# Optimization experiments

Hardware: AMD Instinct MI355X
Metric: run time of the kernel (lower is better)

Reference implementation:

```python
import jax, jax.numpy as jnp
import numpy as np

K = 64
M = 256
V = 5000

def setup_inputs() -> dict:
    key = jax.random.key(0)
    ks = jax.random.split(key, 8)
    feat_x = jax.random.normal(ks[0], (1, V, M), dtype=jnp.float32)
    feat_y = jax.random.normal(ks[1], (1, V, M), dtype=jnp.float32)
    evals_x = jnp.sort(jax.random.uniform(ks[2], (1, K), dtype=jnp.float32))
    evals_y = jnp.sort(jax.random.uniform(ks[3], (1, K), dtype=jnp.float32))
    evecs_trans_x = jax.random.normal(ks[4], (1, K, V), dtype=jnp.float32) / np.sqrt(V)
    evecs_trans_y = jax.random.normal(ks[5], (1, K, V), dtype=jnp.float32) / np.sqrt(V)
    eye = jnp.eye(K, dtype=jnp.float32)
    sqrtMk_x = (eye + 0.05 * jax.random.normal(ks[6], (K, K), dtype=jnp.float32))[None]
    sqrtMk_y = (eye + 0.05 * jax.random.normal(ks[7], (K, K), dtype=jnp.float32))[None]
    return {"feat_x": feat_x, "feat_y": feat_y, "evals_x": evals_x, "evals_y": evals_y,
            "evecs_trans_x": evecs_trans_x, "evecs_trans_y": evecs_trans_y,
            "sqrtMk_x": sqrtMk_x, "sqrtMk_y": sqrtMk_y}

LMBDA = 0.001

def _fmap(fx, fy, ex, ey, tx, ty, sx, sy):
    # squeeze batch dim of 1 (as in torch .squeeze())
    fx, fy = fx[0], fy[0]            # [V, m]
    ex, ey = ex[0], ey[0]            # [k]
    tx, ty = tx[0], ty[0]            # [k, V]
    sx, sy = sx[0], sy[0]            # [k, k]
    A = tx @ fx                      # [k, m] spectral coeffs of feat_x
    B = sy @ (ty @ fy)               # adapt_feature=True: premultiply by sqrtMk_y
    k, m = A.shape
    vec_B = B.T.reshape(m * k, 1)
    At_Ik = jnp.kron(A.T, sy)        # [m*k, k*k] (adapt_feature -> Ik = sqrtMk_y)
    first = At_Ik.T @ At_Ik          # [k^2, k^2]
    # adapt_mask=True branch
    inv_sx = jnp.linalg.inv(sx)
    lx = jnp.diag(ex)
    ly = jnp.diag(ey)
    lx_Ik = jnp.kron(lx @ inv_sx, sy)
    Ik_ly = jnp.kron(inv_sx, sy @ ly)
    Delta = lx_Ik - Ik_ly
    second = Delta.T @ Delta
    rhs = At_Ik.T @ vec_B
    op = first + LMBDA * second
    C = jnp.linalg.solve(op, rhs)
    return C.reshape(k, k).T[None]   # [1, k, k]

def reference(feat_x, feat_y, evals_x, evals_y, evecs_trans_x, evecs_trans_y, sqrtMk_x, sqrtMk_y):
    # bidirectional=False -> only Cxy (Cyx is None in the torch module)
    return _fmap(feat_x, feat_y, evals_x, evals_y, evecs_trans_x, evecs_trans_y, sqrtMk_x, sqrtMk_y)
```

## Files before the change

kernel.cpp:

```cpp
#include <hip/hip_runtime.h>

#define LMBDA 0.001f
#define NS_SY 4
#define NS_SX 5
#define OUTER_FULL 2
#define LDP 68
#define GYS 30

#define WS_A    0
#define WS_FY   16384
#define WS_G1   32768
#define WS_FYAT 36864
#define WS_T1   40960
#define WS_R2   45056
#define WS_R4   49152
#define WS_C    53248
#define WS_FLAGS 57344

#define FMA4(ar, xs, b) { ar[0]=fmaf((xs),(b).x,ar[0]); ar[1]=fmaf((xs),(b).y,ar[1]); \
                          ar[2]=fmaf((xs),(b).z,ar[2]); ar[3]=fmaf((xs),(b).w,ar[3]); }
#define COMP(v,q) ((q)==0?(v).x:((q)==1?(v).y:((q)==2?(v).z:(v).w)))

template<int SA, int SB>
__device__ __forceinline__ void mm64(const float* __restrict__ A,
                                     const float* __restrict__ B,
                                     int ti, int tj, float a[4][4]) {
    #pragma unroll 4
    for (int k = 0; k < 64; k += 4) {
        float4 av0 = *(const float4*)&A[(4 * ti + 0) * SA + k];
        float4 av1 = *(const float4*)&A[(4 * ti + 1) * SA + k];
        float4 av2 = *(const float4*)&A[(4 * ti + 2) * SA + k];
        float4 av3 = *(const float4*)&A[(4 * ti + 3) * SA + k];
        float4 b0 = *(const float4*)&B[(k + 0) * SB + 4 * tj];
        float4 b1 = *(const float4*)&B[(k + 1) * SB + 4 * tj];
        float4 b2 = *(const float4*)&B[(k + 2) * SB + 4 * tj];
        float4 b3 = *(const float4*)&B[(k + 3) * SB + 4 * tj];
        FMA4(a[0], av0.x, b0); FMA4(a[0], av0.y, b1); FMA4(a[0], av0.z, b2); FMA4(a[0], av0.w, b3);
        FMA4(a[1], av1.x, b0); FMA4(a[1], av1.y, b1); FMA4(a[1], av1.z, b2); FMA4(a[1], av1.w, b3);
        FMA4(a[2], av2.x, b0); FMA4(a[2], av2.y, b1); FMA4(a[2], av2.z, b2); FMA4(a[2], av2.w, b3);
        FMA4(a[3], av3.x, b0); FMA4(a[3], av3.y, b1); FMA4(a[3], av3.z, b2); FMA4(a[3], av3.w, b3);
    }
}

template<int SA, int SB>
__device__ __forceinline__ void mmdot(const float* __restrict__ A,
                                      const float* __restrict__ B,
                                      int ti, int tj, float a[4][4]) {
    #pragma unroll 4
    for (int m = 0; m < 64; m += 4) {
        float4 av[4], bv[4];
        #pragma unroll
        for (int r = 0; r < 4; ++r) av[r] = *(const float4*)&A[(4 * ti + r) * SA + m];
        #pragma unroll
        for (int c = 0; c < 4; ++c) bv[c] = *(const float4*)&B[(4 * tj + c) * SB + m];
        #pragma unroll
        for (int r = 0; r < 4; ++r)
            #pragma unroll
            for (int c = 0; c < 4; ++c)
                a[r][c] += av[r].x * bv[c].x + av[r].y * bv[c].y
                         + av[r].z * bv[c].z + av[r].w * bv[c].w;
    }
}

template<int SM>
__device__ __forceinline__ void ns_invert(const float* sM, float* sX, float* sY,
                                          int iters, int ti, int tj,
                                          int tid, float alpha)
{
    const float a2 = alpha * alpha;
    for (int idx = tid; idx < 4096; idx += 256) {
        int i = idx >> 6, j = idx & 63;
        sX[i * LDP + j] = ((i == j) ? 2.f * alpha : 0.f) - a2 * sM[i * SM + j];
    }
    __syncthreads();
    for (int it = 1; it < iters; ++it) {
        float y[4][4] = {};
        mm64<SM, LDP>(sM, sX, ti, tj, y);
        #pragma unroll
        for (int r = 0; r < 4; ++r) {
            float4 v = {y[r][0], y[r][1], y[r][2], y[r][3]};
            *(float4*)&sY[(4 * ti + r) * 64 + 4 * tj] = v;
        }
        __syncthreads();
        float z[4][4] = {};
        mm64<LDP, 64>(sX, sY, ti, tj, z);
        __syncthreads();
        #pragma unroll
        for (int r = 0; r < 4; ++r) {
            float4 xv = *(const float4*)&sX[(4 * ti + r) * LDP + 4 * tj];
            xv.x = 2.f * xv.x - z[r][0];
            xv.y = 2.f * xv.y - z[r][1];
            xv.z = 2.f * xv.z - z[r][2];
            xv.w = 2.f * xv.w - z[r][3];
            *(float4*)&sX[(4 * ti + r) * LDP + 4 * tj] = xv;
        }
        __syncthreads();
    }
}

template<bool DOR>
__device__ __forceinline__ void ns_pass(const float* Xs, const float* Rs,
                                        float* Xd, float* Rd, int ti, int tj)
{
    float xr[4][4] = {}, rr[4][4] = {};
    #pragma unroll 4
    for (int k = 0; k < 64; k += 4) {
        float4 xa[4], ra[4];
        #pragma unroll
        for (int r = 0; r < 4; ++r) {
            xa[r] = *(const float4*)&Xs[(4 * ti + r) * LDP + k];
            if (DOR) ra[r] = *(const float4*)&Rs[(4 * ti + r) * LDP + k];
        }
        #pragma unroll
        for (int q = 0; q < 4; ++q) {
            float4 bv = *(const float4*)&Rs[(k + q) * LDP + 4 * tj];
            #pragma unroll
            for (int r = 0; r < 4; ++r) {
                FMA4(xr[r], COMP(xa[r], q), bv);
                if (DOR) FMA4(rr[r], COMP(ra[r], q), bv);
            }
        }
    }
    #pragma unroll
    for (int r = 0; r < 4; ++r) {
        float4 xo = *(const float4*)&Xs[(4 * ti + r) * LDP + 4 * tj];
        float4 xn = {xo.x + xr[r][0], xo.y + xr[r][1],
                     xo.z + xr[r][2], xo.w + xr[r][3]};
        *(float4*)&Xd[(4 * ti + r) * LDP + 4 * tj] = xn;
        if (DOR) {
            float4 rv = {rr[r][0], rr[r][1], rr[r][2], rr[r][3]};
            *(float4*)&Rd[(4 * ti + r) * LDP + 4 * tj] = rv;
        }
    }
    __syncthreads();
}

__device__ __forceinline__ void wait_ge(int* flag, int target, int tid) {
    if (tid == 0) {
        while (__hip_atomic_load(flag, __ATOMIC_ACQUIRE, __HIP_MEMORY_SCOPE_AGENT) < target)
            __builtin_amdgcn_s_sleep(8);
    }
    __syncthreads();
    __threadfence();
}

__device__ __forceinline__ void signal_one(int* flag, int tid) {
    __syncthreads();
    __threadfence();
    if (tid == 0)
        (void)__hip_atomic_fetch_add(flag, 1, __ATOMIC_RELEASE, __HIP_MEMORY_SCOPE_AGENT);
}

__global__ __launch_bounds__(256, 1) void fused_fmnet(
    const float* __restrict__ fx, const float* __restrict__ fy,
    const float* __restrict__ ex, const float* __restrict__ ey,
    const float* __restrict__ tx, const float* __restrict__ ty,
    const float* __restrict__ sx, const float* __restrict__ sy,
    float* __restrict__ ws, float* __restrict__ out)
{
    extern __shared__ __align__(16) float lds[];
    int* flags = (int*)(ws + WS_FLAGS);
    const int tid = threadIdx.x;
    const int ti = tid >> 4, tj = tid & 15;
    const int bid = blockIdx.x;

    if (bid < 240) {
        float* sT = lds;
        float* sF = lds + 4352;
        const int gx = bid & 7, gy = bid >> 3;
        const int mat = gx >> 2;
        const int m0 = (gx & 3) << 6;
        const float* __restrict__ T = mat ? ty : tx;
        const float* __restrict__ F = mat ? fy : fx;
        float* __restrict__ Out = ws + (mat ? WS_FY : WS_A);

        float4 tv[4], fv[4];
        int sc = gy;
        int vlen = 5000 - (sc << 6); if (vlen > 64) vlen = 64;
        #pragma unroll
        for (int w = 0; w < 4; ++w) {
            const int fidx = tid + (w << 8);
            const int row = fidx >> 4, q = fidx & 15, vv = q << 2;
            if (vv < vlen) tv[w] = *(const float4*)(T + (size_t)row * 5000 + (sc << 6) + vv);
            if (row < vlen) fv[w] = *(const float4*)(F + (size_t)((sc << 6) + row) * 256 + m0 + (q << 2));
        }
        #pragma unroll
        for (int w = 0; w < 4; ++w) {
            const int fidx = tid + (w << 8);
            const int row = fidx >> 4, q = fidx & 15, vv = q << 2;
            if (vv < vlen) {
                sT[(vv + 0) * LDP + row] = tv[w].x;
                sT[(vv + 1) * LDP + row] = tv[w].y;
                sT[(vv + 2) * LDP + row] = tv[w].z;
                sT[(vv + 3) * LDP + row] = tv[w].w;
            }
            if (row < vlen) *(float4*)&sF[row * LDP + (q << 2)] = fv[w];
        }
        __syncthreads();

        float acc[4][4] = {};
        for (;;) {
            const int nsc = sc + GYS;
            int nvlen = 5000 - (nsc << 6);
            if (nvlen > 64) nvlen = 64;
            if (nvlen > 0) {
                #pragma unroll
                for (int w = 0; w < 4; ++w) {
                    const int fidx = tid + (w << 8);
                    const int row = fidx >> 4, q = fidx & 15, vv = q << 2;
                    if (vv < nvlen) tv[w] = *(const float4*)(T + (size_t)row * 5000 + (nsc << 6) + vv);
                    if (row < nvlen) fv[w] = *(const float4*)(F + (size_t)((nsc << 6) + row) * 256 + m0 + (q << 2));
                }
            }
            #pragma unroll 4
            for (int v = 0; v < vlen; ++v) {
                float4 av = *(const float4*)&sT[v * LDP + 4 * ti];
                float4 bv = *(const float4*)&sF[v * LDP + 4 * tj];
                FMA4(acc[0], av.x, bv); FMA4(acc[1], av.y, bv);
                FMA4(acc[2], av.z, bv); FMA4(acc[3], av.w, bv);
            }
            if (nvlen <= 0) break;
            __syncthreads();
            #pragma unroll
            for (int w = 0; w < 4; ++w) {
                const int fidx = tid + (w << 8);
                const int row = fidx >> 4, q = fidx & 15, vv = q << 2;
                if (vv < nvlen) {
                    sT[(vv + 0) * LDP + row] = tv[w].x;
                    sT[(vv + 1) * LDP + row] = tv[w].y;
                    sT[(vv + 2) * LDP + row] = tv[w].z;
                    sT[(vv + 3) * LDP + row] = tv[w].w;
                }
                if (row < nvlen) *(float4*)&sF[row * LDP + (q << 2)] = fv[w];
            }
            __syncthreads();
            sc = nsc; vlen = nvlen;
        }
        #pragma unroll
        for (int r = 0; r < 4; ++r)
            #pragma unroll
            for (int c = 0; c < 4; ++c)
                atomicAdd(&Out[(4 * ti + r) * 256 + m0 + 4 * tj + c], acc[r][c]);
        __syncthreads();
        __threadfence();
        if (tid == 0)
            (void)__hip_atomic_fetch_add(&flags[gx], 1, __ATOMIC_RELEASE, __HIP_MEMORY_SCOPE_AGENT);
    } else if (bid < 244) {
        const int ch = bid - 240;
        wait_ge(&flags[ch], GYS, tid);
        float* sA = lds;
        for (int idx = tid; idx < 1024; idx += 256) {
            int i = idx >> 4, m4 = (idx & 15) << 2;
            *(float4*)&sA[i * LDP + m4] =
                *(const float4*)&ws[WS_A + i * 256 + (ch << 6) + m4];
        }
        __syncthreads();
        float a[4][4] = {};
        mmdot<LDP, LDP>(sA, sA, ti, tj, a);
        #pragma unroll
        for (int r = 0; r < 4; ++r)
            #pragma unroll
            for (int c = 0; c < 4; ++c)
                atomicAdd(&ws[WS_G1 + (4 * ti + r) * 64 + 4 * tj + c], a[r][c]);
        __syncthreads();
        __threadfence();
        if (tid == 0)
            (void)__hip_atomic_fetch_add(&flags[8], 1, __ATOMIC_RELEASE, __HIP_MEMORY_SCOPE_AGENT);
    } else if (bid < 248) {
        const int ch = bid - 244;
        wait_ge(&flags[ch], GYS, tid);
        wait_ge(&flags[4 + ch], GYS, tid);
        float* sFy = lds;
        float* sAx = lds + 4352;
        for (int idx = tid; idx < 1024; idx += 256) {
            int i = idx >> 4, m4 = (idx & 15) << 2;
            *(float4*)&sFy[i * LDP + m4] = *(const float4*)&ws[WS_FY + i * 256 + (ch << 6) + m4];
            *(float4*)&sAx[i * LDP + m4] = *(const float4*)&ws[WS_A  + i * 256 + (ch << 6) + m4];
        }
        __syncthreads();
        float a[4][4] = {};
        mmdot<LDP, LDP>(sFy, sAx, ti, tj, a);
        #pragma unroll
        for (int r = 0; r < 4; ++r)
            #pragma unroll
            for (int c = 0; c < 4; ++c)
                atomicAdd(&ws[WS_FYAT + (4 * ti + r) * 64 + 4 * tj + c], a[r][c]);
        signal_one(&flags[9], tid);
    } else if (bid == 248) {
        float* sSy = lds;
        float* sXx = lds + 4352;
        float* sYy = lds + 8704;
        float* sH  = lds + 12800;
        float* sV  = lds + 16896;
        for (int idx = tid; idx < 1024; idx += 256) {
            int i = idx >> 4, j4 = (idx & 15) << 2;
            *(float4*)&sSy[i * LDP + j4] = *(const float4*)&sy[i * 64 + j4];
        }
        if (tid < 64) sV[tid] = ey[tid];
        __syncthreads();
        {
            float h[4][4] = {};
            for (int k = 0; k < 64; ++k) {
                float4 av = *(const float4*)&sSy[k * LDP + 4 * ti];
                float4 bv = *(const float4*)&sSy[k * LDP + 4 * tj];
                FMA4(h[0], av.x, bv); FMA4(h[1], av.y, bv);
                FMA4(h[2], av.z, bv); FMA4(h[3], av.w, bv);
            }
            #pragma unroll
            for (int r = 0; r < 4; ++r) {
                float4 v = {h[r][0], h[r][1], h[r][2], h[r][3]};
                *(float4*)&sH[(4 * ti + r) * 64 + 4 * tj] = v;
            }
        }
        __syncthreads();
        ns_invert<LDP>(sSy, sXx, sYy, NS_SY, ti, tj, tid, 1.0f);
        {
            float h[4][4] = {};
            mmdot<LDP, LDP>(sXx, sXx, ti, tj, h);
            __syncthreads();
            #pragma unroll
            for (int r = 0; r < 4; ++r) {
                float4 v = {h[r][0], h[r][1], h[r][2], h[r][3]};
                *(float4*)&sSy[(4 * ti + r) * LDP + 4 * tj] = v;
            }
        }
        __syncthreads();
        {
            float a[4][4] = {};
            #pragma unroll 4
            for (int k = 0; k < 64; k += 4) {
                float4 av[4];
                #pragma unroll
                for (int r = 0; r < 4; ++r) av[r] = *(const float4*)&sSy[(4 * ti + r) * LDP + k];
                #pragma unroll
                for (int q = 0; q < 4; ++q) {
                    float e = sV[k + q];
                    float4 bv = *(const float4*)&sH[(k + q) * 64 + 4 * tj];
                    bv.x *= e; bv.y *= e; bv.z *= e; bv.w *= e;
                    #pragma unroll
                    for (int r = 0; r < 4; ++r) FMA4(a[r], COMP(av[r], q), bv);
                }
            }
            #pragma unroll
            for (int r = 0; r < 4; ++r) {
                float4 v = {a[r][0], a[r][1], a[r][2], a[r][3]};
                *(float4*)&ws[WS_C + (4 * ti + r) * 64 + 4 * tj] = v;
            }
        }
        signal_one(&flags[9], tid);
    } else if (bid == 249) {
        float* sM = lds;
        float* sX = lds + 4352;
        float* sY = lds + 8704;
        float* sV = lds + 12800;
        for (int idx = tid; idx < 1024; idx += 256) {
            int i = idx >> 4, j4 = (idx & 15) << 2;
            *(float4*)&sM[i * LDP + j4] = *(const float4*)&sx[i * 64 + j4];
        }
        if (tid < 64) sV[tid] = ex[tid];
        __syncthreads();
        ns_invert<LDP>(sM, sX, sY, NS_SX, ti, tj, tid, 1.0f);
        float aR2[4][4] = {}, aR4[4][4] = {}, aT1[4][4] = {};
        for (int k = 0; k < 64; ++k) {
            float e = sV[k], e2 = e * e;
            float4 av = *(const float4*)&sX[k * LDP + 4 * ti];
            float4 bv = *(const float4*)&sX[k * LDP + 4 * tj];
            float avv[4] = {av.x, av.y, av.z, av.w};
            #pragma unroll
            for (int r = 0; r < 4; ++r) {
                FMA4(aR4[r], avv[r], bv);
                float ea = e * avv[r];
                FMA4(aR2[r], ea, bv);
                float e2a = e2 * avv[r];
                FMA4(aT1[r], e2a, bv);
            }
        }
        #pragma unroll
        for (int r = 0; r < 4; ++r) {
            int o = (4 * ti + r) * 64 + 4 * tj;
            float4 v2 = {aR2[r][0], aR2[r][1], aR2[r][2], aR2[r][3]};
            float4 v4 = {aR4[r][0], aR4[r][1], aR4[r][2], aR4[r][3]};
            float4 v1 = {aT1[r][0], aT1[r][1], aT1[r][2], aT1[r][3]};
            *(float4*)&ws[WS_R2 + o] = v2;
            *(float4*)&ws[WS_R4 + o] = v4;
            *(float4*)&ws[WS_T1 + o] = v1;
        }
        signal_one(&flags[9], tid);
    } else {
        float* sM  = lds;
        float* P1  = lds + 4096;
        float* P2  = lds + 8448;
        float* P3  = lds + 12800;
        float* P4  = lds + 17152;
        float* cR2 = lds + 21504;
        float* cR4 = lds + 25600;

        wait_ge(&flags[8], 4, tid);
        for (int idx = tid; idx < 1024; idx += 256) {
            int i = idx >> 4, j4 = (idx & 15) << 2;
            *(float4*)&sM[i * 64 + j4] = *(const float4*)&ws[WS_G1 + i * 64 + j4];
        }
        __syncthreads();
        if (tid < 64) {
            float s = 0.f;
            for (int j4 = 0; j4 < 64; j4 += 4) {
                float4 v = *(const float4*)&sM[tid * 64 + j4];
                s += v.x * v.x + v.y * v.y + v.z * v.z + v.w * v.w;
            }
            P1[tid] = s;
            P1[64 + tid] = sM[tid * 64 + tid];
        }
        __syncthreads();
        float f2 = 0.f, tr = 0.f;
        for (int i = 0; i < 64; ++i) { f2 += P1[i]; tr += P1[64 + i]; }
        const float alpha = tr / f2, a2 = alpha * alpha;
        for (int idx = tid; idx < 4096; idx += 256) {
            int i = idx >> 6, j = idx & 63;
            float g = sM[i * 64 + j];
            float d = (i == j) ? 1.f : 0.f;
            P3[i * LDP + j] = 2.f * alpha * d - a2 * g;
            P2[i * LDP + j] = d - alpha * g;
        }
        __syncthreads();
        {
            float z[4][4] = {};
            mm64<LDP, LDP>(P2, P2, ti, tj, z);
            #pragma unroll
            for (int r = 0; r < 4; ++r) {
                float4 v = {z[r][0], z[r][1], z[r][2], z[r][3]};
                *(float4*)&P1[(4 * ti + r) * LDP + 4 * tj] = v;
            }
            __syncthreads();
        }
        ns_pass<true >(P3, P1, P4, P2, ti, tj);
        ns_pass<true >(P4, P2, P3, P1, ti, tj);
        ns_pass<true >(P3, P1, P4, P2, ti, tj);
        ns_pass<false>(P4, P2, P3, P3, ti, tj);

        wait_ge(&flags[9], 6, tid);
        for (int idx = tid; idx < 1024; idx += 256) {
            int i = idx >> 4, j4 = (idx & 15) << 2;
            int o = i * 64 + j4;
            float4 gv = *(const float4*)&sM[o];
            float4 t = *(const float4*)&ws[WS_T1 + o];
            gv.x = fmaf(LMBDA, t.x, gv.x); gv.y = fmaf(LMBDA, t.y, gv.y);
            gv.z = fmaf(LMBDA, t.z, gv.z); gv.w = fmaf(LMBDA, t.w, gv.w);
            *(float4*)&sM[o] = gv;
            *(float4*)&cR2[o] = *(const float4*)&ws[WS_R2 + o];
            *(float4*)&cR4[o] = *(const float4*)&ws[WS_R4 + o];
            *(float4*)&P2[i * LDP + j4] = *(const float4*)&ws[WS_C + o];
            *(float4*)&P1[i * LDP + j4] = *(const float4*)&ws[WS_FYAT + o];
        }
        float4 eyv = *(const float4*)&ey[4 * ti];
        float eyr[4] = {eyv.x, eyv.y, eyv.z, eyv.w};
        float leyr[4];
        #pragma unroll
        for (int r = 0; r < 4; ++r) leyr[r] = LMBDA * eyr[r];

        float fyr[4][4], xreg[4][4];
        #pragma unroll
        for (int r = 0; r < 4; ++r) {
            float4 v = *(const float4*)&ws[WS_FYAT + (4 * ti + r) * 64 + 4 * tj];
            fyr[r][0] = v.x; fyr[r][1] = v.y; fyr[r][2] = v.z; fyr[r][3] = v.w;
        }
        __syncthreads();

        {
            float dX[4][4] = {};
            mm64<LDP, LDP>(P1, P3, ti, tj, dX);
            #pragma unroll
            for (int r = 0; r < 4; ++r) {
                #pragma unroll
                for (int c = 0; c < 4; ++c) xreg[r][c] = dX[r][c];
                float4 v = {xreg[r][0], xreg[r][1], xreg[r][2], xreg[r][3]};
                *(float4*)&P4[(4 * ti + r) * LDP + 4 * tj] = v;
            }
        }
        __syncthreads();

        float E1[4][4];
        for (int it = 0; it < OUTER_FULL; ++it) {
            {
                float Sm[4][4] = {}, S2[4][4] = {}, S4[4][4] = {};
                #pragma unroll 2
                for (int k = 0; k < 64; k += 4) {
                    float4 av[4];
                    #pragma unroll
                    for (int r = 0; r < 4; ++r)
                        av[r] = *(const float4*)&P4[(4 * ti + r) * LDP + k];
                    #pragma unroll
                    for (int q = 0; q < 4; ++q) {
                        float4 mv = *(const float4*)&sM[(k + q) * 64 + 4 * tj];
                        float4 qv = *(const float4*)&cR2[(k + q) * 64 + 4 * tj];
                        float4 rv = *(const float4*)&cR4[(k + q) * 64 + 4 * tj];
                        #pragma unroll
                        for (int r = 0; r < 4; ++r) {
                            float x = COMP(av[r], q);
                            FMA4(Sm[r], x, mv);
                            FMA4(S2[r], x, qv);
                            FMA4(S4[r], x, rv);
                        }
                    }
                }
                __syncthreads();
                #pragma unroll
                for (int r = 0; r < 4; ++r) {
                    float4 e2;
                    e2.x = LMBDA * fmaf(eyr[r], S4[r][0], -S2[r][0]);
                    e2.y = LMBDA * fmaf(eyr[r], S4[r][1], -S2[r][1]);
                    e2.z = LMBDA * fmaf(eyr[r], S4[r][2], -S2[r][2]);
                    e2.w = LMBDA * fmaf(eyr[r], S4[r][3], -S2[r][3]);
                    *(float4*)&P1[(4 * ti + r) * LDP + 4 * tj] = e2;
                    #pragma unroll
                    for (int c = 0; c < 4; ++c)
                        E1[r][c] = fmaf(-leyr[r], S2[r][c], Sm[r][c]);
                }
            }
            __syncthreads();
            {
                float Z[4][4] = {};
                mm64<LDP, LDP>(P2, P1, ti, tj, Z);
                __syncthreads();
                #pragma unroll
                for (int r = 0; r < 4; ++r) {
                    float4 w;
                    w.x = fyr[r][0] - E1[r][0] - Z[r][0];
                    w.y = fyr[r][1] - E1[r][1] - Z[r][1];
                    w.z = fyr[r][2] - E1[r][2] - Z[r][2];
                    w.w = fyr[r][3] - E1[r][3] - Z[r][3];
                    *(float4*)&P1[(4 * ti + r) * LDP + 4 * tj] = w;
                }
            }
            __syncthreads();
            {
                float dX[4][4] = {};
                mm64<LDP, LDP>(P1, P3, ti, tj, dX);
                #pragma unroll
                for (int r = 0; r < 4; ++r) {
                    float4 v;
                    #pragma unroll
                    for (int c = 0; c < 4; ++c) xreg[r][c] += dX[r][c];
                    v.x = xreg[r][0]; v.y = xreg[r][1]; v.z = xreg[r][2]; v.w = xreg[r][3];
                    *(float4*)&P4[(4 * ti + r) * LDP + 4 * tj] = v;
                    if (it == OUTER_FULL - 1)
                        *(float4*)&out[(4 * ti + r) * 64 + 4 * tj] = v;
                }
            }
            if (it == OUTER_FULL - 1) break;
            __syncthreads();
        }
    }
}

extern "C" void kernel_launch(void* const* d_in, const int* in_sizes, int n_in,
                              void* d_out, int out_size, void* d_ws, size_t ws_size,
                              hipStream_t stream) {
    (void)in_sizes; (void)n_in; (void)out_size; (void)ws_size;
    const float* fx = (const float*)d_in[0];
    const float* fy = (const float*)d_in[1];
    const float* ex = (const float*)d_in[2];
    const float* ey = (const float*)d_in[3];
    const float* tx = (const float*)d_in[4];
    const float* ty = (const float*)d_in[5];
    const float* sx = (const float*)d_in[6];
    const float* sy = (const float*)d_in[7];
    float* ws = (float*)d_ws;
    float* out = (float*)d_out;

    (void)hipFuncSetAttribute((const void*)fused_fmnet,
                              hipFuncAttributeMaxDynamicSharedMemorySize, 134144);

    (void)hipMemsetAsync(d_ws, 0, (size_t)(WS_T1) * sizeof(float), stream);
    (void)hipMemsetAsync((char*)d_ws + (size_t)WS_FLAGS * sizeof(float), 0, 64, stream);
    fused_fmnet<<<251, 256, 134144, stream>>>(fx, fy, ex, ey, tx, ty, sx, sy, ws, out);
}
```

Before: 170.6 us.

## Rebalance projection blocks between A and Fy, halve-thread serial solver matmuls

The projection stage now gives 160 blocks with stride 40 to the A (tx·fx) product and 76 blocks with stride 19 to the Fy product, replacing a uniform 30-block split, and renumbers the downstream role blocks. The serial solver block runs several 64x64 matmuls on 128 threads with 4x8 register tiles instead of 256 threads with 4x4 tiles. E1 is stored to LDS rather than kept in registers so it can be read under the new thread mapping. This aims to balance the streaming work and cut instruction or sync overhead on the latency-bound tail, at the cost of leaving half the threads idle in those matmuls.

After: 184.8 us. 1.08x slower.

```diff
diff --git a/kernel.cpp b/kernel.cpp
--- a/kernel.cpp
+++ b/kernel.cpp
@@ -5,7 +5,8 @@
 #define NS_SX 5
 #define OUTER_FULL 2
 #define LDP 68
-#define GYS 30
+#define GYS_A 40
+#define GYS_F 19
 
 #define WS_A    0
 #define WS_FY   16384
@@ -43,6 +44,29 @@
 }
 
 template<int SA, int SB>
+__device__ __forceinline__ void mm64h(const float* __restrict__ A,
+                                      const float* __restrict__ B,
+                                      int ti, int tj, float a[4][8]) {
+    #pragma unroll 4
+    for (int k = 0; k < 64; k += 4) {
+        float4 av[4];
+        #pragma unroll
+        for (int r = 0; r < 4; ++r) av[r] = *(const float4*)&A[(4 * ti + r) * SA + k];
+        #pragma unroll
+        for (int q = 0; q < 4; ++q) {
+            float4 b0 = *(const float4*)&B[(k + q) * SB + 8 * tj];
+            float4 b1 = *(const float4*)&B[(k + q) * SB + 8 * tj + 4];
+            #pragma unroll
+            for (int r = 0; r < 4; ++r) {
+                float x = COMP(av[r], q);
+                FMA4(a[r], x, b0);
+                FMA4((a[r] + 4), x, b1);
+            }
+        }
+    }
+}
+
+template<int SA, int SB>
 __device__ __forceinline__ void mmdot(const float* __restrict__ A,
                                       const float* __restrict__ B,
                                       int ti, int tj, float a[4][4]) {
@@ -98,9 +122,8 @@
     }
 }
 
-template<bool DOR>
-__device__ __forceinline__ void ns_pass(const float* Xs, const float* Rs,
-                                        float* Xd, float* Rd, int ti, int tj)
+__device__ __forceinline__ void ns_pass_d(const float* Xs, const float* Rs,
+                                          float* Xd, float* Rd, int ti, int tj)
 {
     float xr[4][4] = {}, rr[4][4] = {};
     #pragma unroll 4
@@ -109,7 +132,7 @@
         #pragma unroll
         for (int r = 0; r < 4; ++r) {
             xa[r] = *(const float4*)&Xs[(4 * ti + r) * LDP + k];
-            if (DOR) ra[r] = *(const float4*)&Rs[(4 * ti + r) * LDP + k];
+            ra[r] = *(const float4*)&Rs[(4 * ti + r) * LDP + k];
         }
         #pragma unroll
         for (int q = 0; q < 4; ++q) {
@@ -117,7 +140,7 @@
             #pragma unroll
             for (int r = 0; r < 4; ++r) {
                 FMA4(xr[r], COMP(xa[r], q), bv);
-                if (DOR) FMA4(rr[r], COMP(ra[r], q), bv);
+                FMA4(rr[r], COMP(ra[r], q), bv);
             }
         }
     }
@@ -127,10 +150,8 @@
         float4 xn = {xo.x + xr[r][0], xo.y + xr[r][1],
                      xo.z + xr[r][2], xo.w + xr[r][3]};
         *(float4*)&Xd[(4 * ti + r) * LDP + 4 * tj] = xn;
-        if (DOR) {
-            float4 rv = {rr[r][0], rr[r][1], rr[r][2], rr[r][3]};
-            *(float4*)&Rd[(4 * ti + r) * LDP + 4 * tj] = rv;
-        }
+        float4 rv = {rr[r][0], rr[r][1], rr[r][2], rr[r][3]};
+        *(float4*)&Rd[(4 * ti + r) * LDP + 4 * tj] = rv;
     }
     __syncthreads();
 }
@@ -164,12 +185,13 @@
     const int ti = tid >> 4, tj = tid & 15;
     const int bid = blockIdx.x;
 
-    if (bid < 240) {
+    if (bid < 236) {
         float* sT = lds;
         float* sF = lds + 4352;
-        const int gx = bid & 7, gy = bid >> 3;
-        const int mat = gx >> 2;
-        const int m0 = (gx & 3) << 6;
+        int mat, gx, gy, gstride;
+        if (bid < 160) { mat = 0; gx = bid & 3; gy = bid >> 2; gstride = GYS_A; }
+        else { int b2 = bid - 160; mat = 1; gx = b2 & 3; gy = b2 >> 2; gstride = GYS_F; }
+        const int m0 = gx << 6;
         const float* __restrict__ T = mat ? ty : tx;
         const float* __restrict__ F = mat ? fy : fx;
         float* __restrict__ Out = ws + (mat ? WS_FY : WS_A);
@@ -200,7 +222,7 @@
 
         float acc[4][4] = {};
         for (;;) {
-            const int nsc = sc + GYS;
+            const int nsc = sc + gstride;
             int nvlen = 5000 - (nsc << 6);
             if (nvlen > 64) nvlen = 64;
             if (nvlen > 0) {
@@ -244,10 +266,10 @@
         __syncthreads();
         __threadfence();
         if (tid == 0)
-            (void)__hip_atomic_fetch_add(&flags[gx], 1, __ATOMIC_RELEASE, __HIP_MEMORY_SCOPE_AGENT);
-    } else if (bid < 244) {
-        const int ch = bid - 240;
-        wait_ge(&flags[ch], GYS, tid);
+            (void)__hip_atomic_fetch_add(&flags[mat * 4 + gx], 1, __ATOMIC_RELEASE, __HIP_MEMORY_SCOPE_AGENT);
+    } else if (bid < 240) {
+        const int ch = bid - 236;
+        wait_ge(&flags[ch], GYS_A, tid);
         float* sA = lds;
         for (int idx = tid; idx < 1024; idx += 256) {
             int i = idx >> 4, m4 = (idx & 15) << 2;
@@ -266,10 +288,10 @@
         __threadfence();
         if (tid == 0)
             (void)__hip_atomic_fetch_add(&flags[8], 1, __ATOMIC_RELEASE, __HIP_MEMORY_SCOPE_AGENT);
-    } else if (bid < 248) {
-        const int ch = bid - 244;
-        wait_ge(&flags[ch], GYS, tid);
-        wait_ge(&flags[4 + ch], GYS, tid);
+    } else if (bid < 244) {
+        const int ch = bid - 240;
+        wait_ge(&flags[ch], GYS_A, tid);
+        wait_ge(&flags[4 + ch], GYS_F, tid);
         float* sFy = lds;
         float* sAx = lds + 4352;
         for (int idx = tid; idx < 1024; idx += 256) {
@@ -286,7 +308,7 @@
             for (int c = 0; c < 4; ++c)
                 atomicAdd(&ws[WS_FYAT + (4 * ti + r) * 64 + 4 * tj + c], a[r][c]);
         signal_one(&flags[9], tid);
-    } else if (bid == 248) {
+    } else if (bid == 244) {
         float* sSy = lds;
         float* sXx = lds + 4352;
         float* sYy = lds + 8704;
@@ -348,7 +370,7 @@
             }
         }
         signal_one(&flags[9], tid);
-    } else if (bid == 249) {
+    } else if (bid == 245) {
         float* sM = lds;
         float* sX = lds + 4352;
         float* sY = lds + 8704;
@@ -394,6 +416,7 @@
         float* P4  = lds + 17152;
         float* cR2 = lds + 21504;
         float* cR4 = lds + 25600;
+        const int ti2 = tid >> 3, tj2 = tid & 7;
 
         wait_ge(&flags[8], 4, tid);
         for (int idx = tid; idx < 1024; idx += 256) {
@@ -422,21 +445,32 @@
             P2[i * LDP + j] = d - alpha * g;
         }
         __syncthreads();
-        {
-            float z[4][4] = {};
-            mm64<LDP, LDP>(P2, P2, ti, tj, z);
-            #pragma unroll
-            for (int r = 0; r < 4; ++r) {
-                float4 v = {z[r][0], z[r][1], z[r][2], z[r][3]};
-                *(float4*)&P1[(4 * ti + r) * LDP + 4 * tj] = v;
-            }
-            __syncthreads();
-        }
-        ns_pass<true >(P3, P1, P4, P2, ti, tj);
-        ns_pass<true >(P4, P2, P3, P1, ti, tj);
-        ns_pass<true >(P3, P1, P4, P2, ti, tj);
-        ns_pass<false>(P4, P2, P3, P3, ti, tj);
-
+        if (tid < 128) {
+            float z[4][8] = {};
+            mm64h<LDP, LDP>(P2, P2, ti2, tj2, z);
+            #pragma unroll
+            for (int r = 0; r < 4; ++r) {
+                *(float4*)&P1[(4 * ti2 + r) * LDP + 8 * tj2]     = *(float4*)&z[r][0];
+                *(float4*)&P1[(4 * ti2 + r) * LDP + 8 * tj2 + 4] = *(float4*)&z[r][4];
+            }
+        }
+        __syncthreads();
+        ns_pass_d(P3, P1, P4, P2, ti, tj);
+        ns_pass_d(P4, P2, P3, P1, ti, tj);
+        ns_pass_d(P3, P1, P4, P2, ti, tj);
+        if (tid < 128) {
+            float z[4][8] = {};
+            mm64h<LDP, LDP>(P4, P2, ti2, tj2, z);
+            #pragma unroll
+            for (int r = 0; r < 4; ++r) {
+                float4 x0 = *(const float4*)&P4[(4 * ti2 + r) * LDP + 8 * tj2];
+                float4 x1 = *(const float4*)&P4[(4 * ti2 + r) * LDP + 8 * tj2 + 4];
+                x0.x += z[r][0]; x0.y += z[r][1]; x0.z += z[r][2]; x0.w += z[r][3];
+                x1.x += z[r][4]; x1.y += z[r][5]; x1.z += z[r][6]; x1.w += z[r][7];
+                *(float4*)&P3[(4 * ti2 + r) * LDP + 8 * tj2]     = x0;
+                *(float4*)&P3[(4 * ti2 + r) * LDP + 8 * tj2 + 4] = x1;
+            }
+        }
         wait_ge(&flags[9], 6, tid);
         for (int idx = tid; idx < 1024; idx += 256) {
             int i = idx >> 4, j4 = (idx & 15) << 2;
@@ -456,29 +490,29 @@
         float leyr[4];
         #pragma unroll
         for (int r = 0; r < 4; ++r) leyr[r] = LMBDA * eyr[r];
-
-        float fyr[4][4], xreg[4][4];
-        #pragma unroll
-        for (int r = 0; r < 4; ++r) {
-            float4 v = *(const float4*)&ws[WS_FYAT + (4 * ti + r) * 64 + 4 * tj];
-            fyr[r][0] = v.x; fyr[r][1] = v.y; fyr[r][2] = v.z; fyr[r][3] = v.w;
-        }
-        __syncthreads();
-
-        {
-            float dX[4][4] = {};
-            mm64<LDP, LDP>(P1, P3, ti, tj, dX);
+        float fyr[4][8], xreg[4][8];
+        if (tid < 128) {
+            #pragma unroll
+            for (int r = 0; r < 4; ++r) {
+                *(float4*)&fyr[r][0] = *(const float4*)&ws[WS_FYAT + (4 * ti2 + r) * 64 + 8 * tj2];
+                *(float4*)&fyr[r][4] = *(const float4*)&ws[WS_FYAT + (4 * ti2 + r) * 64 + 8 * tj2 + 4];
+            }
+        }
+        __syncthreads();
+
+        if (tid < 128) {
+            float dX[4][8] = {};
+            mm64h<LDP, LDP>(P1, P3, ti2, tj2, dX);
             #pragma unroll
             for (int r = 0; r < 4; ++r) {
                 #pragma unroll
-                for (int c = 0; c < 4; ++c) xreg[r][c] = dX[r][c];
-                float4 v = {xreg[r][0], xreg[r][1], xreg[r][2], xreg[r][3]};
-                *(float4*)&P4[(4 * ti + r) * LDP + 4 * tj] = v;
-            }
-        }
-        __syncthreads();
-
-        float E1[4][4];
+                for (int c = 0; c < 8; ++c) xreg[r][c] = dX[r][c];
+                *(float4*)&P4[(4 * ti2 + r) * LDP + 8 * tj2]     = *(float4*)&xreg[r][0];
+                *(float4*)&P4[(4 * ti2 + r) * LDP + 8 * tj2 + 4] = *(float4*)&xreg[r][4];
+            }
+        }
+        __syncthreads();
+
         for (int it = 0; it < OUTER_FULL; ++it) {
             {
                 float Sm[4][4] = {}, S2[4][4] = {}, S4[4][4] = {};
@@ -505,45 +539,56 @@
                 __syncthreads();
                 #pragma unroll
                 for (int r = 0; r < 4; ++r) {
-                    float4 e2;
+                    float4 e2, e1;
                     e2.x = LMBDA * fmaf(eyr[r], S4[r][0], -S2[r][0]);
                     e2.y = LMBDA * fmaf(eyr[r], S4[r][1], -S2[r][1]);
                     e2.z = LMBDA * fmaf(eyr[r], S4[r][2], -S2[r][2]);
                     e2.w = LMBDA * fmaf(eyr[r], S4[r][3], -S2[r][3]);
                     *(float4*)&P1[(4 * ti + r) * LDP + 4 * tj] = e2;
-                    #pragma unroll
-                    for (int c = 0; c < 4; ++c)
-                        E1[r][c] = fmaf(-leyr[r], S2[r][c], Sm[r][c]);
+                    e1.x = fmaf(-leyr[r], S2[r][0], Sm[r][0]);
+                    e1.y = fmaf(-leyr[r], S2[r][1], Sm[r][1]);
+                    e1.z = fmaf(-leyr[r], S2[r][2], Sm[r][2]);
+                    e1.w = fmaf(-leyr[r], S2[r][3], Sm[r][3]);
+                    *(float4*)&P4[(4 * ti + r) * LDP + 4 * tj] = e1;
                 }
             }
             __syncthreads();
-            {
-                float Z[4][4] = {};
-                mm64<LDP, LDP>(P2, P1, ti, tj, Z);
-                __syncthreads();
+            float Z[4][8] = {};
+            if (tid < 128)
+                mm64h<LDP, LDP>(P2, P1, ti2, tj2, Z);
+            __syncthreads();
+            if (tid < 128) {
                 #pragma unroll
                 for (int r = 0; r < 4; ++r) {
-                    float4 w;
-                    w.x = fyr[r][0] - E1[r][0] - Z[r][0];
-                    w.y = fyr[r][1] - E1[r][1] - Z[r][1];
-                    w.z = fyr[r][2] - E1[r][2] - Z[r][2];
-                    w.w = fyr[r][3] - E1[r][3] - Z[r][3];
-                    *(float4*)&P1[(4 * ti + r) * LDP + 4 * tj] = w;
+                    float4 e10 = *(const float4*)&P4[(4 * ti2 + r) * LDP + 8 * tj2];
+                    float4 e11 = *(const float4*)&P4[(4 * ti2 + r) * LDP + 8 * tj2 + 4];
+                    float4 w0, w1;
+                    w0.x = fyr[r][0] - e10.x - Z[r][0];
+                    w0.y = fyr[r][1] - e10.y - Z[r][1];
+                    w0.z = fyr[r][2] - e10.z - Z[r][2];
+                    w0.w = fyr[r][3] - e10.w - Z[r][3];
+                    w1.x = fyr[r][4] - e11.x - Z[r][4];
+                    w1.y = fyr[r][5] - e11.y - Z[r][5];
+                    w1.z = fyr[r][6] - e11.z - Z[r][6];
+                    w1.w = fyr[r][7] - e11.w - Z[r][7];
+                    *(float4*)&P1[(4 * ti2 + r) * LDP + 8 * tj2]     = w0;
+                    *(float4*)&P1[(4 * ti2 + r) * LDP + 8 * tj2 + 4] = w1;
                 }
             }
             __syncthreads();
-            {
-                float dX[4][4] = {};
-                mm64<LDP, LDP>(P1, P3, ti, tj, dX);
+            if (tid < 128) {
+                float dX[4][8] = {};
+                mm64h<LDP, LDP>(P1, P3, ti2, tj2, dX);
                 #pragma unroll
                 for (int r = 0; r < 4; ++r) {
-                    float4 v;
                     #pragma unroll
-                    for (int c = 0; c < 4; ++c) xreg[r][c] += dX[r][c];
-                    v.x = xreg[r][0]; v.y = xreg[r][1]; v.z = xreg[r][2]; v.w = xreg[r][3];
-                    *(float4*)&P4[(4 * ti + r) * LDP + 4 * tj] = v;
-                    if (it == OUTER_FULL - 1)
-                        *(float4*)&out[(4 * ti + r) * 64 + 4 * tj] = v;
+                    for (int c = 0; c < 8; ++c) xreg[r][c] += dX[r][c];
+                    *(float4*)&P4[(4 * ti2 + r) * LDP + 8 * tj2]     = *(float4*)&xreg[r][0];
+                    *(float4*)&P4[(4 * ti2 + r) * LDP + 8 * tj2 + 4] = *(float4*)&xreg[r][4];
+                    if (it == OUTER_FULL - 1) {
+                        *(float4*)&out[(4 * ti2 + r) * 64 + 8 * tj2]     = *(float4*)&xreg[r][0];
+                        *(float4*)&out[(4 * ti2 + r) * 64 + 8 * tj2 + 4] = *(float4*)&xreg[r][4];
+                    }
                 }
             }
             if (it == OUTER_FULL - 1) break;
@@ -572,5 +617,5 @@
 
     (void)hipMemsetAsync(d_ws, 0, (size_t)(WS_T1) * sizeof(float), stream);
     (void)hipMemsetAsync((char*)d_ws + (size_t)WS_FLAGS * sizeof(float), 0, 64, stream);
-    fused_fmnet<<<251, 256, 134144, stream>>>(fx, fy, ex, ey, tx, ty, sx, sy, ws, out);
-}
+    fused_fmnet<<<247, 256, 134144, stream>>>(fx, fy, ex, ey, tx, ty, sx, sy, ws, out);
+}
```
